# Kernel optimization log

Measured on AMD Instinct MI355X. Metric: run time of the kernel, lower is better.

Reference implementation:

```python
import jax, jax.numpy as jnp
import numpy as np

H, W = 16, 16
DIM = 512
HEADS = 8
DIM_HEAD = 64
INNER = HEADS * DIM_HEAD  # 512
B = 8
N = H * W  # 256
SCALE = DIM_HEAD ** -0.5
EPS = 1e-5


def _index_map(h, w):
    # index_map[n, m] = dx * (2w-1) + dy with dx = x-i+h-1, dy = y-j+w-1
    xs = np.arange(h)
    ys = np.arange(w)
    dx = xs[:, None] - xs[None, :] + h - 1            # (h, h)
    dy = ys[:, None] - ys[None, :] + w - 1            # (w, w)
    idx = dx[:, None, :, None] * (2 * w - 1) + dy[None, :, None, :]  # (h, w, h, w)
    return idx.reshape(h * w, h * w).astype(np.int32)


def setup_inputs() -> dict:
    key = jax.random.key(0)
    ks = jax.random.split(key, 5)
    x = jax.random.normal(ks[0], (B, N, DIM), dtype=jnp.float32)
    ln_g = jnp.ones((DIM,), jnp.float32)
    ln_b = jnp.zeros((DIM,), jnp.float32)
    w_qkv = jax.random.normal(ks[1], (DIM, 3 * INNER), jnp.float32) * 0.02
    unique_params = jax.random.normal(ks[2], ((2 * H - 1) * (2 * W - 1), INNER), jnp.float32) * 0.02
    w_out = jax.random.normal(ks[3], (INNER, DIM), jnp.float32) * 0.02
    b_out = jnp.zeros((DIM,), jnp.float32)
    idx_map = jnp.asarray(_index_map(H, W))  # (N, N) int32
    return {"x": x, "ln_g": ln_g, "ln_b": ln_b, "w_qkv": w_qkv,
            "unique_params": unique_params, "w_out": w_out, "b_out": b_out,
            "idx_map": idx_map}


def reference(x, ln_g, ln_b, w_qkv, unique_params, w_out, b_out, idx_map):
    b, n, _ = x.shape
    # LayerNorm
    mu = jnp.mean(x, axis=-1, keepdims=True)
    var = jnp.mean(jnp.square(x - mu), axis=-1, keepdims=True)
    xn = (x - mu) * jax.lax.rsqrt(var + EPS) * ln_g + ln_b
    # qkv projection (no bias)
    qkv = xn @ w_qkv                                  # (b, n, 3*inner)
    q, k, v = jnp.split(qkv, 3, axis=-1)
    q = q.reshape(b, n, HEADS, DIM_HEAD)
    k = k.reshape(b, n, HEADS, DIM_HEAD)
    v = v.reshape(b, n, HEADS, DIM_HEAD)
    # attention scores
    dots = jnp.einsum('bnhd,bmhd->bhnm', q, k) * SCALE
    attn = jax.nn.softmax(dots, axis=-1)              # (b, h, n, m)
    # relative-position table: (n, m, h, d)
    rpos = unique_params[idx_map].reshape(n, n, HEADS, DIM_HEAD)
    # out[b,h,n,d] = sum_m attn[b,h,n,m] * (v[b,m,h,d] + rpos[n,m,h,d])
    out = jnp.einsum('bhnm,bmhd->bnhd', attn, v) \
        + jnp.einsum('bhnm,nmhd->bnhd', attn, rpos)
    out = out.reshape(b, n, INNER)
    return out @ w_out + b_out
```

## Files before the change

### kernel.cpp

```cpp
#include <hip/hip_runtime.h>
#include <math.h>

#define NB 8
#define SEQ 256
#define DIMC 512
#define NHEAD 8
#define DHEAD 64
#define SCALEF 0.125f

typedef __attribute__((ext_vector_type(8))) short s16x8;
typedef __attribute__((ext_vector_type(4))) float f32x4;

typedef __attribute__((address_space(3))) unsigned int lds_u32_t;
typedef const __attribute__((address_space(1))) unsigned int g_u32_t;
static __device__ __forceinline__ void gl_lds16(const void* gsrc, void* ldst) {
  __builtin_amdgcn_global_load_lds((g_u32_t*)gsrc, (lds_u32_t*)ldst, 16, 0, 0);
}

static __device__ __forceinline__ unsigned short f2bf(float f) {
  union { float f; unsigned u; } c; c.f = f;
  unsigned r = c.u + 0x7FFF + ((c.u >> 16) & 1);
  return (unsigned short)(r >> 16);
}

static __device__ void tcast_body(const float* __restrict__ W,
    unsigned short* __restrict__ WT, int K, int N, int n0, int k0, int t,
    float (*tile)[65]) {
#pragma unroll
  for (int i = 0; i < 16; ++i) {
    const int idx = i * 256 + t;
    const int kl = idx >> 6, nl = idx & 63;
    tile[kl][nl] = W[(size_t)(k0 + kl) * N + n0 + nl];
  }
  __syncthreads();
#pragma unroll
  for (int i = 0; i < 16; ++i) {
    const int idx = i * 256 + t;
    const int nl = idx >> 6, kl = idx & 63;
    WT[(size_t)(n0 + nl) * K + k0 + kl] = f2bf(tile[kl][nl]);
  }
}

__global__ __launch_bounds__(256) void prep_kernel(const float* __restrict__ x,
    const float* __restrict__ g, const float* __restrict__ bta,
    const float* __restrict__ w_qkv, const float* __restrict__ w_out,
    const float* __restrict__ up, unsigned short* __restrict__ xnb,
    unsigned short* __restrict__ wqt, unsigned short* __restrict__ wot,
    unsigned short* __restrict__ upT) {
  __shared__ float tile[64][65];
  __shared__ float sh_s[4], sh_q[4];
  const int t = threadIdx.x;
  const int bid = blockIdx.x;
  if (bid < 192) {
    tcast_body(w_qkv, wqt, 512, 1536, (bid % 24) * 64, (bid / 24) * 64, t, tile);
  } else if (bid < 256) {
    const int b2 = bid - 192;
    tcast_body(w_out, wot, 512, 512, (b2 % 8) * 64, (b2 / 8) * 64, t, tile);
  } else if (bid < 384) {
    const int b2 = bid - 256;
    const int k0 = (b2 >> 3) * 64, n0 = (b2 & 7) * 64;
#pragma unroll
    for (int i = 0; i < 16; ++i) {
      const int idx = i * 256 + t;
      const int kl = idx >> 6, nl = idx & 63;
      const int k = k0 + kl;
      tile[kl][nl] = (k < 961) ? up[(size_t)k * 512 + n0 + nl] : 0.0f;
    }
    __syncthreads();
#pragma unroll
    for (int i = 0; i < 16; ++i) {
      const int idx = i * 256 + t;
      const int nl = idx >> 6, kl = idx & 63;
      if (k0 + kl < 992)
        upT[(size_t)(n0 + nl) * 992 + k0 + kl] = f2bf(tile[kl][nl]);
    }
  } else {
    const int row = bid - 384;
    const float2 v = ((const float2*)(x + (size_t)row * DIMC))[t];
    float s = v.x + v.y;
    float q = v.x * v.x + v.y * v.y;
#pragma unroll
    for (int off = 32; off > 0; off >>= 1) {
      s += __shfl_down(s, off);
      q += __shfl_down(q, off);
    }
    const int wave = t >> 6, lane = t & 63;
    if (lane == 0) { sh_s[wave] = s; sh_q[wave] = q; }
    __syncthreads();
    const float fs = sh_s[0] + sh_s[1] + sh_s[2] + sh_s[3];
    const float fq = sh_q[0] + sh_q[1] + sh_q[2] + sh_q[3];
    const float mean = fs * (1.0f / DIMC);
    const float inv = rsqrtf(fq * (1.0f / DIMC) - mean * mean + 1e-5f);
    const float2 gv = ((const float2*)g)[t];
    const float2 bv = ((const float2*)bta)[t];
    ushort2 o;
    o.x = f2bf((v.x - mean) * inv * gv.x + bv.x);
    o.y = f2bf((v.y - mean) * inv * gv.y + bv.y);
    ((ushort2*)(xnb + (size_t)row * DIMC))[t] = o;
  }
}

template <int BM, int BN, bool BIAS, bool OUTBF, bool VSPLIT>
__global__ __launch_bounds__(256) void mfma_gemm_bt(
    const unsigned short* __restrict__ A, const unsigned short* __restrict__ BT,
    const float* __restrict__ bias, void* __restrict__ Cv,
    unsigned short* __restrict__ vtb, int M, int K, int N) {
  constexpr int TR = BM / 32;
  constexpr int TC = BN / 32;
  __shared__ unsigned short As[2][BM * 64];
  __shared__ unsigned short Bs[2][BN * 64];
  const int t = threadIdx.x;
  const int wave = t >> 6, lane = t & 63;
  const int wr = wave >> 1, wc = wave & 1;
  const int bm = blockIdx.x * BM, bn = blockIdx.y * BN;
  const int fr = lane & 15, q4 = lane >> 4;

  f32x4 acc[TR][TC] = {};

  const int nk = K >> 6;

#define STAGE_TILE(sel, kb)                                                   \
  {                                                                           \
    const int k0s = (kb) << 6;                                                \
    _Pragma("unroll")                                                         \
    for (int c = 0; c < BM * 8 / 256; ++c) {                                  \
      const int p = c * 256 + t;                                              \
      const int row = p >> 3;                                                 \
      const int so = (p & 7) ^ (row & 7);                                     \
      gl_lds16(A + (size_t)(bm + row) * K + k0s + so * 8,                     \
               &As[sel][(size_t)(c * 256 + wave * 64) * 8]);                  \
    }                                                                         \
    _Pragma("unroll")                                                         \
    for (int c = 0; c < BN * 8 / 256; ++c) {                                  \
      const int p = c * 256 + t;                                              \
      const int row = p >> 3;                                                 \
      const int so = (p & 7) ^ (row & 7);                                     \
      gl_lds16(BT + (size_t)(bn + row) * K + k0s + so * 8,                    \
               &Bs[sel][(size_t)(c * 256 + wave * 64) * 8]);                  \
    }                                                                         \
  }

  STAGE_TILE(0, 0);
  __syncthreads();
  int cur = 0;
  for (int kb = 0; kb < nk; ++kb) {
    if (kb + 1 < nk) STAGE_TILE(cur ^ 1, kb + 1);
    s16x8 af[2][TR], bfr[2][TC];
#pragma unroll
    for (int ks = 0; ks < 2; ++ks) {
#pragma unroll
      for (int i = 0; i < TR; ++i) {
        const int row = wr * (BM / 2) + i * 16 + fr;
        const int op = (ks * 4 + q4) ^ (row & 7);
        af[ks][i] = *(const s16x8*)(&As[cur][row * 64 + op * 8]);
      }
#pragma unroll
      for (int j = 0; j < TC; ++j) {
        const int row = wc * (BN / 2) + j * 16 + fr;
        const int op = (ks * 4 + q4) ^ (row & 7);
        bfr[ks][j] = *(const s16x8*)(&Bs[cur][row * 64 + op * 8]);
      }
    }
#pragma unroll
    for (int ks = 0; ks < 2; ++ks)
#pragma unroll
      for (int i = 0; i < TR; ++i)
#pragma unroll
        for (int j = 0; j < TC; ++j)
          acc[i][j] = __builtin_amdgcn_mfma_f32_16x16x32_bf16(
              af[ks][i], bfr[ks][j], acc[i][j], 0, 0, 0);
    __syncthreads();
    cur ^= 1;
  }
#undef STAGE_TILE

  if (VSPLIT && bn >= 1024) {
#pragma unroll
    for (int i = 0; i < TR; ++i) {
#pragma unroll
      for (int j = 0; j < TC; ++j) {
        const int hc = bn - 1024 + wc * (BN / 2) + j * 16 + fr;
        const int h = hc >> 6, d = hc & 63;
#pragma unroll
        for (int r = 0; r < 4; ++r) {
          const int row = bm + wr * (BM / 2) + i * 16 + q4 * 4 + r;
          const int b = row >> 8, m = row & 255;
          vtb[(size_t)((b * 8 + h) * 64 + d) * 256 + m] = f2bf(acc[i][j][r]);
        }
      }
    }
    return;
  }
#pragma unroll
  for (int i = 0; i < TR; ++i) {
#pragma unroll
    for (int j = 0; j < TC; ++j) {
      const int col = bn + wc * (BN / 2) + j * 16 + fr;
      const float bv = BIAS ? bias[col] : 0.0f;
#pragma unroll
      for (int r = 0; r < 4; ++r) {
        const int row = bm + wr * (BM / 2) + i * 16 + q4 * 4 + r;
        if constexpr (OUTBF) {
          ((unsigned short*)Cv)[(size_t)row * N + col] = f2bf(acc[i][j][r] + bv);
        } else {
          ((float*)Cv)[(size_t)row * N + col] = acc[i][j][r] + bv;
        }
      }
    }
  }
}

#define PSTR 264
#define ASTR2 520
__global__ __launch_bounds__(256) void attn_rpos_kernel(
    const unsigned short* __restrict__ qkvb,
    const unsigned short* __restrict__ vtb,
    const unsigned short* __restrict__ upT,
    unsigned short* __restrict__ ob) {
  __shared__ unsigned short ascat[16 * ASTR2];
  __shared__ unsigned short p_lds[16 * PSTR];
  __shared__ float smax[4][16], ssum[4][16];
  const int bh = blockIdx.y, b = bh >> 3, h = bh & 7;
  const int xn = blockIdx.x;
  const int n0 = xn * 16;
  const int t = threadIdx.x, wave = t >> 6, lane = t & 63;
  const int fr = lane & 15, q4 = lane >> 4;
  const int kwin0 = (xn * 31) & ~7;

  {
    const s16x8 z = {0, 0, 0, 0, 0, 0, 0, 0};
#pragma unroll
    for (int i = 0; i < 5; ++i) {
      const int idx = i * 256 + t;
      if (idx < 16 * ASTR2 / 8) *(s16x8*)(ascat + idx * 8) = z;
    }
  }

  s16x8 qf[2];
  {
    const size_t qrow = (size_t)(b * SEQ + n0 + fr) * 1536 + h * 64;
#pragma unroll
    for (int ks = 0; ks < 2; ++ks)
      qf[ks] = *(const s16x8*)(qkvb + qrow + ks * 32 + q4 * 8);
  }

  f32x4 s[4];
#pragma unroll
  for (int j = 0; j < 4; ++j) s[j] = (f32x4){0.f, 0.f, 0.f, 0.f};
  {
    const unsigned short* kb =
        qkvb + (size_t)(b * SEQ + wave * 64 + fr) * 1536 + 512 + h * 64;
#pragma unroll
    for (int ks = 0; ks < 2; ++ks)
#pragma unroll
      for (int j = 0; j < 4; ++j) {
        const s16x8 kf =
            *(const s16x8*)(kb + (size_t)j * (16 * 1536) + ks * 32 + q4 * 8);
        s[j] = __builtin_amdgcn_mfma_f32_16x16x32_bf16(qf[ks], kf, s[j], 0, 0, 0);
      }
  }

  float mx[4] = {-1e30f, -1e30f, -1e30f, -1e30f};
#pragma unroll
  for (int j = 0; j < 4; ++j)
#pragma unroll
    for (int r = 0; r < 4; ++r) {
      s[j][r] *= SCALEF;
      mx[r] = fmaxf(mx[r], s[j][r]);
    }
#pragma unroll
  for (int r = 0; r < 4; ++r) {
    mx[r] = fmaxf(mx[r], __shfl_xor(mx[r], 1));
    mx[r] = fmaxf(mx[r], __shfl_xor(mx[r], 2));
    mx[r] = fmaxf(mx[r], __shfl_xor(mx[r], 4));
    mx[r] = fmaxf(mx[r], __shfl_xor(mx[r], 8));
  }
  if (fr == 0) {
#pragma unroll
    for (int r = 0; r < 4; ++r) smax[wave][q4 * 4 + r] = mx[r];
  }
  __syncthreads();

  float fm[4];
#pragma unroll
  for (int r = 0; r < 4; ++r) {
    const int row = q4 * 4 + r;
    fm[r] = fmaxf(fmaxf(smax[0][row], smax[1][row]),
                  fmaxf(smax[2][row], smax[3][row]));
  }
  float sum[4] = {0.f, 0.f, 0.f, 0.f};
#pragma unroll
  for (int j = 0; j < 4; ++j)
#pragma unroll
    for (int r = 0; r < 4; ++r) {
      s[j][r] = __expf(s[j][r] - fm[r]);
      sum[r] += s[j][r];
    }
#pragma unroll
  for (int r = 0; r < 4; ++r) {
    sum[r] += __shfl_xor(sum[r], 1);
    sum[r] += __shfl_xor(sum[r], 2);
    sum[r] += __shfl_xor(sum[r], 4);
    sum[r] += __shfl_xor(sum[r], 8);
  }
  if (fr == 0) {
#pragma unroll
    for (int r = 0; r < 4; ++r) ssum[wave][q4 * 4 + r] = sum[r];
  }
  __syncthreads();

  float invs[4];
#pragma unroll
  for (int r = 0; r < 4; ++r) {
    const int row = q4 * 4 + r;
    invs[r] = 1.0f / (ssum[0][row] + ssum[1][row] + ssum[2][row] + ssum[3][row]);
  }

#pragma unroll
  for (int j = 0; j < 4; ++j) {
    const int mt = wave * 4 + j;
#pragma unroll
    for (int r = 0; r < 4; ++r) {
      const int row = q4 * 4 + r;
      const unsigned short pb = f2bf(s[j][r] * invs[r]);
      p_lds[row * PSTR + mt * 16 + fr] = pb;
      const int c = (xn - mt + 15) * 31 + (row - fr + 15) - kwin0;
      ascat[row * ASTR2 + c] = pb;
    }
  }
  __syncthreads();

  f32x4 oA = (f32x4){0.f, 0.f, 0.f, 0.f}, oB = oA, oC = oA, oD = oA;
  {
    const unsigned short* uB =
        upT + (size_t)(h * 64 + wave * 16 + fr) * 992 + kwin0;
    const unsigned short* aR = ascat + fr * ASTR2;
#pragma unroll
    for (int ks = 0; ks < 8; ++ks) {
      const s16x8 af = *(const s16x8*)(aR + ks * 32 + q4 * 8);
      const s16x8 bfg = *(const s16x8*)(uB + ks * 32 + q4 * 8);
      oA = __builtin_amdgcn_mfma_f32_16x16x32_bf16(af, bfg, oA, 0, 0, 0);
    }
#pragma unroll
    for (int ks = 8; ks < 16; ++ks) {
      const s16x8 af = *(const s16x8*)(aR + ks * 32 + q4 * 8);
      const s16x8 bfg = *(const s16x8*)(uB + ks * 32 + q4 * 8);
      oB = __builtin_amdgcn_mfma_f32_16x16x32_bf16(af, bfg, oB, 0, 0, 0);
    }
  }
  {
    const unsigned short* vB = vtb + (size_t)(bh * 64 + wave * 16 + fr) * 256;
    const unsigned short* pR = p_lds + fr * PSTR;
#pragma unroll
    for (int ks = 0; ks < 4; ++ks) {
      const s16x8 pf = *(const s16x8*)(pR + ks * 32 + q4 * 8);
      const s16x8 vfg = *(const s16x8*)(vB + ks * 32 + q4 * 8);
      oC = __builtin_amdgcn_mfma_f32_16x16x32_bf16(pf, vfg, oC, 0, 0, 0);
    }
#pragma unroll
    for (int ks = 4; ks < 8; ++ks) {
      const s16x8 pf = *(const s16x8*)(pR + ks * 32 + q4 * 8);
      const s16x8 vfg = *(const s16x8*)(vB + ks * 32 + q4 * 8);
      oD = __builtin_amdgcn_mfma_f32_16x16x32_bf16(pf, vfg, oD, 0, 0, 0);
    }
  }
  const f32x4 o = (oA + oB) + (oC + oD);
#pragma unroll
  for (int r = 0; r < 4; ++r) {
    const int n = n0 + q4 * 4 + r;
    ob[(size_t)(b * SEQ + n) * DIMC + h * 64 + wave * 16 + fr] = f2bf(o[r]);
  }
}

extern "C" void kernel_launch(void* const* d_in, const int* in_sizes, int n_in,
                              void* d_out, int out_size, void* d_ws,
                              size_t ws_size, hipStream_t stream) {
  const float* x = (const float*)d_in[0];
  const float* ln_g = (const float*)d_in[1];
  const float* ln_b = (const float*)d_in[2];
  const float* w_qkv = (const float*)d_in[3];
  const float* up = (const float*)d_in[4];
  const float* w_out = (const float*)d_in[5];
  const float* b_out = (const float*)d_in[6];
  float* out = (float*)d_out;

  unsigned short* u = (unsigned short*)d_ws;
  unsigned short* qkvb = u;
  unsigned short* xnb = u + 3145728;
  unsigned short* ob = u + 4194304;
  unsigned short* wqt = u + 5242880;
  unsigned short* wot = u + 6029312;
  unsigned short* upT = u + 6291456;
  unsigned short* vtb = u + 6799360;
  if (ws_size < (size_t)7847936 * sizeof(unsigned short)) return;

  prep_kernel<<<2432, 256, 0, stream>>>(x, ln_g, ln_b, w_qkv, w_out, up,
                                        xnb, wqt, wot, upT);
  mfma_gemm_bt<64, 64, false, true, true>
      <<<dim3(32, 24), 256, 0, stream>>>(xnb, wqt, nullptr, qkvb, vtb,
                                         2048, 512, 1536);
  attn_rpos_kernel<<<dim3(16, 64), 256, 0, stream>>>(qkvb, vtb, upT, ob);
  mfma_gemm_bt<64, 32, true, false, false>
      <<<dim3(32, 16), 256, 0, stream>>>(ob, wot, b_out, out, nullptr,
                                         2048, 512, 512);
}
```

Baseline: 108.2 us.

## Vectorize LayerNorm rows per wave, pack V-transpose stores, raise MFMA priority

The LayerNorm part of the prep kernel now handles 8 rows per block, with each wave normalizing two rows using float4 loads, xor-shuffle reductions, and 16-byte bf16 stores. This removes the shared-memory reduction and barrier and cuts the LayerNorm grid from 2048 to 256 blocks. The V-transpose epilogue in the QKV GEMM writes four consecutive bf16 values as one ushort4 instead of four scalar stores. The attention kernel wraps its MFMA loops in s_setprio to raise wave priority during matrix work; this could help or hurt scheduling.

```diff
diff --git a/kernel.cpp b/kernel.cpp
--- a/kernel.cpp
+++ b/kernel.cpp
@@ -1,11 +1,8 @@
 #include <hip/hip_runtime.h>
 #include <math.h>
 
-#define NB 8
 #define SEQ 256
 #define DIMC 512
-#define NHEAD 8
-#define DHEAD 64
 #define SCALEF 0.125f
 
 typedef __attribute__((ext_vector_type(8))) short s16x8;
@@ -48,7 +45,6 @@
     unsigned short* __restrict__ wqt, unsigned short* __restrict__ wot,
     unsigned short* __restrict__ upT) {
   __shared__ float tile[64][65];
-  __shared__ float sh_s[4], sh_q[4];
   const int t = threadIdx.x;
   const int bid = blockIdx.x;
   if (bid < 192) {
@@ -75,28 +71,39 @@
         upT[(size_t)(n0 + nl) * 992 + k0 + kl] = f2bf(tile[kl][nl]);
     }
   } else {
-    const int row = bid - 384;
-    const float2 v = ((const float2*)(x + (size_t)row * DIMC))[t];
-    float s = v.x + v.y;
-    float q = v.x * v.x + v.y * v.y;
-#pragma unroll
-    for (int off = 32; off > 0; off >>= 1) {
-      s += __shfl_down(s, off);
-      q += __shfl_down(q, off);
-    }
+    const int r8 = (bid - 384) * 8;
     const int wave = t >> 6, lane = t & 63;
-    if (lane == 0) { sh_s[wave] = s; sh_q[wave] = q; }
-    __syncthreads();
-    const float fs = sh_s[0] + sh_s[1] + sh_s[2] + sh_s[3];
-    const float fq = sh_q[0] + sh_q[1] + sh_q[2] + sh_q[3];
-    const float mean = fs * (1.0f / DIMC);
-    const float inv = rsqrtf(fq * (1.0f / DIMC) - mean * mean + 1e-5f);
-    const float2 gv = ((const float2*)g)[t];
-    const float2 bv = ((const float2*)bta)[t];
-    ushort2 o;
-    o.x = f2bf((v.x - mean) * inv * gv.x + bv.x);
-    o.y = f2bf((v.y - mean) * inv * gv.y + bv.y);
-    ((ushort2*)(xnb + (size_t)row * DIMC))[t] = o;
+    const int d0 = lane * 8;
+    const float4 g0 = *(const float4*)(g + d0);
+    const float4 g1 = *(const float4*)(g + d0 + 4);
+    const float4 b0 = *(const float4*)(bta + d0);
+    const float4 b1 = *(const float4*)(bta + d0 + 4);
+#pragma unroll
+    for (int rr = 0; rr < 2; ++rr) {
+      const int row = r8 + wave * 2 + rr;
+      const float4 v0 = *(const float4*)(x + (size_t)row * DIMC + d0);
+      const float4 v1 = *(const float4*)(x + (size_t)row * DIMC + d0 + 4);
+      float s = v0.x + v0.y + v0.z + v0.w + v1.x + v1.y + v1.z + v1.w;
+      float q = v0.x * v0.x + v0.y * v0.y + v0.z * v0.z + v0.w * v0.w +
+                v1.x * v1.x + v1.y * v1.y + v1.z * v1.z + v1.w * v1.w;
+#pragma unroll
+      for (int off = 1; off < 64; off <<= 1) {
+        s += __shfl_xor(s, off);
+        q += __shfl_xor(q, off);
+      }
+      const float mean = s * (1.0f / DIMC);
+      const float inv = rsqrtf(q * (1.0f / DIMC) - mean * mean + 1e-5f);
+      s16x8 o;
+      o[0] = (short)f2bf((v0.x - mean) * inv * g0.x + b0.x);
+      o[1] = (short)f2bf((v0.y - mean) * inv * g0.y + b0.y);
+      o[2] = (short)f2bf((v0.z - mean) * inv * g0.z + b0.z);
+      o[3] = (short)f2bf((v0.w - mean) * inv * g0.w + b0.w);
+      o[4] = (short)f2bf((v1.x - mean) * inv * g1.x + b1.x);
+      o[5] = (short)f2bf((v1.y - mean) * inv * g1.y + b1.y);
+      o[6] = (short)f2bf((v1.z - mean) * inv * g1.z + b1.z);
+      o[7] = (short)f2bf((v1.w - mean) * inv * g1.w + b1.w);
+      *(s16x8*)(xnb + (size_t)row * DIMC + d0) = o;
+    }
   }
 }
 
@@ -181,12 +188,12 @@
       for (int j = 0; j < TC; ++j) {
         const int hc = bn - 1024 + wc * (BN / 2) + j * 16 + fr;
         const int h = hc >> 6, d = hc & 63;
-#pragma unroll
-        for (int r = 0; r < 4; ++r) {
-          const int row = bm + wr * (BM / 2) + i * 16 + q4 * 4 + r;
-          const int b = row >> 8, m = row & 255;
-          vtb[(size_t)((b * 8 + h) * 64 + d) * 256 + m] = f2bf(acc[i][j][r]);
-        }
+        const int row = bm + wr * (BM / 2) + i * 16 + q4 * 4;
+        const int b = row >> 8, m = row & 255;
+        ushort4 w;
+        w.x = f2bf(acc[i][j][0]); w.y = f2bf(acc[i][j][1]);
+        w.z = f2bf(acc[i][j][2]); w.w = f2bf(acc[i][j][3]);
+        *(ushort4*)&vtb[(size_t)((b * 8 + h) * 64 + d) * 256 + m] = w;
       }
     }
     return;
@@ -250,6 +257,7 @@
   {
     const unsigned short* kb =
         qkvb + (size_t)(b * SEQ + wave * 64 + fr) * 1536 + 512 + h * 64;
+    __builtin_amdgcn_s_setprio(1);
 #pragma unroll
     for (int ks = 0; ks < 2; ++ks)
 #pragma unroll
@@ -258,6 +266,7 @@
             *(const s16x8*)(kb + (size_t)j * (16 * 1536) + ks * 32 + q4 * 8);
         s[j] = __builtin_amdgcn_mfma_f32_16x16x32_bf16(qf[ks], kf, s[j], 0, 0, 0);
       }
+    __builtin_amdgcn_s_setprio(0);
   }
 
   float mx[4] = {-1e30f, -1e30f, -1e30f, -1e30f};
@@ -335,6 +344,7 @@
     const unsigned short* uB =
         upT + (size_t)(h * 64 + wave * 16 + fr) * 992 + kwin0;
     const unsigned short* aR = ascat + fr * ASTR2;
+    __builtin_amdgcn_s_setprio(1);
 #pragma unroll
     for (int ks = 0; ks < 8; ++ks) {
       const s16x8 af = *(const s16x8*)(aR + ks * 32 + q4 * 8);
@@ -347,10 +357,12 @@
       const s16x8 bfg = *(const s16x8*)(uB + ks * 32 + q4 * 8);
       oB = __builtin_amdgcn_mfma_f32_16x16x32_bf16(af, bfg, oB, 0, 0, 0);
     }
+    __builtin_amdgcn_s_setprio(0);
   }
   {
     const unsigned short* vB = vtb + (size_t)(bh * 64 + wave * 16 + fr) * 256;
     const unsigned short* pR = p_lds + fr * PSTR;
+    __builtin_amdgcn_s_setprio(1);
 #pragma unroll
     for (int ks = 0; ks < 4; ++ks) {
       const s16x8 pf = *(const s16x8*)(pR + ks * 32 + q4 * 8);
@@ -363,6 +375,7 @@
       const s16x8 vfg = *(const s16x8*)(vB + ks * 32 + q4 * 8);
       oD = __builtin_amdgcn_mfma_f32_16x16x32_bf16(pf, vfg, oD, 0, 0, 0);
     }
+    __builtin_amdgcn_s_setprio(0);
   }
   const f32x4 o = (oA + oB) + (oC + oD);
 #pragma unroll
@@ -394,8 +407,8 @@
   unsigned short* vtb = u + 6799360;
   if (ws_size < (size_t)7847936 * sizeof(unsigned short)) return;
 
-  prep_kernel<<<2432, 256, 0, stream>>>(x, ln_g, ln_b, w_qkv, w_out, up,
-                                        xnb, wqt, wot, upT);
+  prep_kernel<<<640, 256, 0, stream>>>(x, ln_g, ln_b, w_qkv, w_out, up,
+                                       xnb, wqt, wot, upT);
   mfma_gemm_bt<64, 64, false, true, true>
       <<<dim3(32, 24), 256, 0, stream>>>(xnb, wqt, nullptr, qkvb, vtb,
                                          2048, 512, 1536);
```

New measurement: 108.1 us. About the same (-0.1%).
